# Performance work log

Measured on AMD Instinct MI355X. Metric: run time of the kernel, lower is better.

The kernel has to match this reference:

```python
import jax, jax.numpy as jnp
import numpy as np

B, n, A = 64, 1024, 32          # graphs, nodes/graph, actions/graph
N = B * n
EH = 2048                        # undirected edges per graph
HID, H = 128, 4
C = HID // H
NF, EF, AD, NI, L = 1, 1, 7, 4, 3
NEG_SLOPE = 0.2


def setup_inputs() -> dict:
    ks = jax.random.split(jax.random.key(0), 16)
    x = jax.random.normal(ks[0], (N, NF), jnp.float32)
    s = jax.random.randint(ks[1], (B, EH), 0, n)
    d = jax.random.randint(ks[2], (B, EH), 0, n)
    off = (jnp.arange(B) * n)[:, None]
    s = (s + off).reshape(-1)
    d = (d + off).reshape(-1)
    # bidirectional edges (unrooted trees): both i->j and j->i
    edge_index = jnp.stack([jnp.concatenate([s, d]), jnp.concatenate([d, s])]).astype(jnp.int32)
    E = edge_index.shape[1]
    edge_attr = jax.random.uniform(ks[3], (E, EF), jnp.float32)
    idx = jax.random.randint(ks[4], (B, A, NI), 0, n).astype(jnp.float32)
    meta = jax.random.normal(ks[5], (B, A, AD - NI), jnp.float32)
    action_tensor = jnp.concatenate([idx, meta], axis=-1)
    batch_idx = jnp.repeat(jnp.arange(B, dtype=jnp.int32), n)
    batch_ptr = jnp.arange(B + 1, dtype=jnp.int32) * n

    def lin(k, i, o):
        return jax.random.normal(k, (i, o), jnp.float32) / np.float32(np.sqrt(i))

    inp = dict(x=x, edge_attr=edge_attr, action_tensor=action_tensor,
               edge_index=edge_index, batch_idx=batch_idx, batch_ptr=batch_ptr)
    inp["Wn"] = lin(ks[6], NF, HID); inp["bn"] = jnp.zeros((HID,), jnp.float32)
    kl = jax.random.split(ks[7], 4 * L)
    inp["gWl"] = jnp.stack([lin(kl[i], HID, HID) for i in range(L)])
    inp["gWr"] = jnp.stack([lin(kl[L + i], HID, HID) for i in range(L)])
    inp["gWe"] = jnp.stack([lin(kl[2 * L + i], EF, HID) for i in range(L)])
    inp["gatt"] = jnp.stack([jax.random.normal(kl[3 * L + i], (H, C), jnp.float32) * 0.1 for i in range(L)])
    inp["gbl"] = jnp.zeros((L, HID), jnp.float32)
    inp["gbr"] = jnp.zeros((L, HID), jnp.float32)
    inp["gb"] = jnp.zeros((L, HID), jnp.float32)
    mlp_in = NI * HID + (AD - NI)
    inp["aW1"] = lin(ks[8], mlp_in, HID); inp["ab1"] = jnp.zeros((HID,), jnp.float32)
    inp["aW2"] = lin(ks[9], HID, HID); inp["ab2"] = jnp.zeros((HID,), jnp.float32)
    inp["qW1"] = lin(ks[10], 4 * HID, HID); inp["qb1"] = jnp.zeros((HID,), jnp.float32)
    inp["qW2"] = lin(ks[11], HID, HID); inp["qb2"] = jnp.zeros((HID,), jnp.float32)
    inp["qW3"] = lin(ks[12], HID, 1); inp["qb3"] = jnp.zeros((1,), jnp.float32)
    return inp


def _gatv2(h, src, dst, ea, Wl, bl, Wr, br, We, att, b):
    # PyG GATv2Conv: e_ij = att . leaky_relu(lin_l(x_j) + lin_r(x_i) + lin_edge(e_ij))
    Nn = h.shape[0]
    xl = (h @ Wl + bl).reshape(Nn, H, C)   # source transform
    xr = (h @ Wr + br).reshape(Nn, H, C)   # target transform
    ee = (ea @ We).reshape(-1, H, C)       # edge transform (no bias in PyG)
    e = jax.nn.leaky_relu(xl[src] + xr[dst] + ee, NEG_SLOPE)   # [E,H,C]
    logits = jnp.einsum('ehc,hc->eh', e, att)
    m = jax.ops.segment_max(logits, dst, num_segments=Nn)       # stable softmax per target node
    ex = jnp.exp(logits - m[dst])
    alpha = ex / jax.ops.segment_sum(ex, dst, num_segments=Nn)[dst]
    msg = (xl[src] * alpha[:, :, None]).reshape(-1, HID)
    return jax.ops.segment_sum(msg, dst, num_segments=Nn) + b


def reference(x, edge_attr, action_tensor, Wn, bn, gWl, gbl, gWr, gbr, gWe, gatt, gb,
              aW1, ab1, aW2, ab2, qW1, qb1, qW2, qb2, qW3, qb3,
              edge_index, batch_idx, batch_ptr):
    Nn = x.shape[0]
    nb = batch_ptr.shape[0] - 1
    # GATv2Conv default add_self_loops=True, fill_value='mean' for edge_attr
    loops = jnp.arange(Nn, dtype=edge_index.dtype)
    src = jnp.concatenate([edge_index[0], loops])
    dst = jnp.concatenate([edge_index[1], loops])
    ea = jnp.concatenate([edge_attr, jnp.broadcast_to(edge_attr.mean(0), (Nn, edge_attr.shape[1]))], 0)
    h = jax.nn.relu(x @ Wn + bn)
    for l in range(L):
        h = jax.nn.relu(_gatv2(h, src, dst, ea, gWl[l], gbl[l], gWr[l], gbr[l], gWe[l], gatt[l], gb[l])) + h
    # sum / mean / max pooling per graph
    sums = jax.ops.segment_sum(h, batch_idx, num_segments=nb)
    cnt = jax.ops.segment_sum(jnp.ones((Nn, 1), h.dtype), batch_idx, num_segments=nb)
    means = sums / cnt
    maxs = jax.ops.segment_max(h, batch_idx, num_segments=nb)
    tree_emb = jnp.concatenate([sums, means, maxs], -1)          # [B, 3*HID]
    # action encoding: gather node embeddings at action node indices (shifted by batch_ptr)
    ni = action_tensor[..., :NI].astype(jnp.int32) + batch_ptr[:-1][:, None, None]
    g = h[ni].reshape(nb, action_tensor.shape[1], NI * HID)
    ai = jnp.concatenate([g, action_tensor[..., NI:]], -1)
    ae = jax.nn.relu(jax.nn.relu(ai @ aW1 + ab1) @ aW2 + ab2)    # [B, A, HID]
    comb = jnp.concatenate([jnp.broadcast_to(tree_emb[:, None, :], (nb, ae.shape[1], 3 * HID)), ae], -1)
    q = jax.nn.relu(comb @ qW1 + qb1)
    q = jax.nn.relu(q @ qW2 + qb2)
    return (q @ qW3 + qb3).squeeze(-1)                            # [B, A]
```

## Files before the change

kernel.cpp:

```cpp
#include <hip/hip_runtime.h>
#include <hip/hip_bf16.h>

#define NNODES 65536
#define NGRAPH 64
#define NPG 1024
#define NACT 32
#define HID 128
#define DEGS 32

typedef __attribute__((ext_vector_type(8))) short bf16x8;
typedef __attribute__((ext_vector_type(4))) float f32x4;

__device__ __forceinline__ void load8(float* dst, const float* src) {
    float4 q0 = ((const float4*)src)[0];
    float4 q1 = ((const float4*)src)[1];
    dst[0]=q0.x; dst[1]=q0.y; dst[2]=q0.z; dst[3]=q0.w;
    dst[4]=q1.x; dst[5]=q1.y; dst[6]=q1.z; dst[7]=q1.w;
}

__device__ __forceinline__ void load8bf(float* dst, const unsigned short* src) {
    uint4 q = *(const uint4*)src;
    unsigned int u0 = q.x, u1 = q.y, u2 = q.z, u3 = q.w;
    dst[0] = __uint_as_float(u0 << 16); dst[1] = __uint_as_float(u0 & 0xffff0000u);
    dst[2] = __uint_as_float(u1 << 16); dst[3] = __uint_as_float(u1 & 0xffff0000u);
    dst[4] = __uint_as_float(u2 << 16); dst[5] = __uint_as_float(u2 & 0xffff0000u);
    dst[6] = __uint_as_float(u3 << 16); dst[7] = __uint_as_float(u3 & 0xffff0000u);
}

__device__ __forceinline__ unsigned short f2bf(float f) {
    unsigned int u = __float_as_uint(f);
    u = (u + 0x7fffu + ((u >> 16) & 1u)) >> 16;
    return (unsigned short)u;
}

__global__ void setup_k(const int* __restrict__ ei, const float* __restrict__ ea,
                        int* __restrict__ cursor, float* __restrict__ meansum,
                        int2* __restrict__ csr, int E0, int nsb,
                        const float* __restrict__ gWl, const float* __restrict__ gWr,
                        unsigned short* __restrict__ wtl, unsigned short* __restrict__ wtr,
                        const float* __restrict__ aW1, const float* __restrict__ aW2,
                        const float* __restrict__ qW1, const float* __restrict__ qW2,
                        unsigned short* __restrict__ wA1t, unsigned short* __restrict__ wA2t,
                        unsigned short* __restrict__ wQ1t, unsigned short* __restrict__ wQ2t) {
    int bid = blockIdx.x, t = threadIdx.x;
    if (bid < nsb) {
        __shared__ float s[256];
        int e = bid * 256 + t;
        float v = 0.f;
        if (e < E0) {
            int sn = ei[e], d = ei[E0 + e];
            int pos = atomicAdd(&cursor[d], 1);
            if (pos >= DEGS) pos = DEGS - 1;
            csr[(size_t)d * DEGS + pos] = make_int2(sn, __float_as_int(ea[e]));
            v = ea[e];
        }
        s[t] = v; __syncthreads();
        for (int off = 128; off > 0; off >>= 1) { if (t < off) s[t] += s[t+off]; __syncthreads(); }
        if (t == 0) atomicAdd(meansum, s[0]);
    } else if (bid < nsb + 192) {
        int idx = (bid - nsb) * 256 + t;
        int l = idx >> 14, rem = idx & 16383;
        int n = rem >> 7, k = rem & 127;
        int src = l*16384 + k*128 + n;
        wtl[idx] = f2bf(gWl[src]);
        wtr[idx] = f2bf(gWr[src]);
    } else {
        int n = bid - nsb - 192;
        for (int k = t; k < 544; k += 256)
            wA1t[n*544 + k] = (k < 515) ? f2bf(aW1[(size_t)k*128 + n]) : (unsigned short)0;
        if (t < 128) {
            wA2t[n*128 + t] = f2bf(aW2[(size_t)t*128 + n]);
            wQ1t[n*128 + t] = f2bf(qW1[(size_t)(384 + t)*128 + n]);
            wQ2t[n*128 + t] = f2bf(qW2[(size_t)t*128 + n]);
        }
    }
}

__global__ __launch_bounds__(256) void gemm_lr_mfma_k(
    const unsigned short* __restrict__ hb, const float* __restrict__ x,
    const float* __restrict__ Wn, const float* __restrict__ bn, int l0,
    const unsigned short* __restrict__ wtl, const unsigned short* __restrict__ wtr,
    const float* __restrict__ bl, const float* __restrict__ br,
    unsigned short* __restrict__ xlb, unsigned short* __restrict__ xrb) {
    int wave = threadIdx.x >> 6;
    int lane = threadIdx.x & 63;
    int lr = lane & 15;
    int lq = lane >> 4;
    int r0 = blockIdx.x * 128 + wave * 32;

    bf16x8 a[2][4];
    if (l0) {
        float xv0 = x[r0 + lr], xv1 = x[r0 + 16 + lr];
#pragma unroll
        for (int kf = 0; kf < 4; ++kf) {
            float wn[8], bv[8];
            load8(wn, Wn + kf*32 + lq*8);
            load8(bv, bn + kf*32 + lq*8);
            union { bf16x8 v; unsigned short u[8]; } p0, p1;
#pragma unroll
            for (int j = 0; j < 8; ++j) {
                p0.u[j] = f2bf(fmaxf(fmaf(xv0, wn[j], bv[j]), 0.f));
                p1.u[j] = f2bf(fmaxf(fmaf(xv1, wn[j], bv[j]), 0.f));
            }
            a[0][kf] = p0.v; a[1][kf] = p1.v;
        }
    } else {
        const short* hs = (const short*)hb;
#pragma unroll
        for (int rt = 0; rt < 2; ++rt)
#pragma unroll
            for (int kf = 0; kf < 4; ++kf)
                a[rt][kf] = *(const bf16x8*)(hs + (size_t)(r0 + rt*16 + lr)*HID + kf*32 + lq*8);
    }

    const short* ws[2]   = {(const short*)wtl, (const short*)wtr};
    const float* bias[2] = {bl, br};
    unsigned short* outp[2] = {xlb, xrb};

#pragma unroll
    for (int m = 0; m < 2; ++m) {
        const short* W = ws[m];
        f32x4 acc[2][8];
#pragma unroll
        for (int rt = 0; rt < 2; ++rt)
#pragma unroll
            for (int ct = 0; ct < 8; ++ct) acc[rt][ct] = (f32x4){0.f,0.f,0.f,0.f};

        bf16x8 b[4], nb[4];
#pragma unroll
        for (int kf = 0; kf < 4; ++kf)
            b[kf] = *(const bf16x8*)(W + (size_t)(lr)*HID + kf*32 + lq*8);
#pragma unroll
        for (int ct = 0; ct < 8; ++ct) {
            if (ct < 7) {
#pragma unroll
                for (int kf = 0; kf < 4; ++kf)
                    nb[kf] = *(const bf16x8*)(W + (size_t)((ct+1)*16 + lr)*HID + kf*32 + lq*8);
            }
#pragma unroll
            for (int rt = 0; rt < 2; ++rt)
#pragma unroll
                for (int kf = 0; kf < 4; ++kf)
                    acc[rt][ct] = __builtin_amdgcn_mfma_f32_16x16x32_bf16(a[rt][kf], b[kf], acc[rt][ct], 0, 0, 0);
#pragma unroll
            for (int kf = 0; kf < 4; ++kf) b[kf] = nb[kf];
        }
#pragma unroll
        for (int ct = 0; ct < 8; ++ct) {
            float bv = bias[m][ct*16 + lr];
#pragma unroll
            for (int rt = 0; rt < 2; ++rt)
#pragma unroll
                for (int rg = 0; rg < 4; ++rg) {
                    int row = r0 + rt*16 + lq*4 + rg;
                    outp[m][(size_t)row*HID + ct*16 + lr] = f2bf(acc[rt][ct][rg] + bv);
                }
        }
    }
}

__global__ __launch_bounds__(256, 4) void gat_edge_k(
    const unsigned short* __restrict__ xlb, const unsigned short* __restrict__ xrb,
    float* __restrict__ h, unsigned short* __restrict__ hb,
    const int* __restrict__ deg, const int2* __restrict__ csr,
    const float* __restrict__ We, const float* __restrict__ att,
    const float* __restrict__ gb, const float* __restrict__ meansum, float inv_e0,
    const float* __restrict__ x, const float* __restrict__ Wn, const float* __restrict__ bn,
    int l0, int do_pool, float* __restrict__ tree_sum, float* __restrict__ tree_max) {
    __shared__ float ps[16][132];
    __shared__ float pm[16][132];
    int xcd  = blockIdx.x & 7;
    int slot = blockIdx.x >> 3;
    int g    = xcd * 8 + (slot >> 6);
    int j    = slot & 63;
    int t    = threadIdx.x;
    int nd   = t >> 4;
    int v    = g * NPG + j * 16 + nd;
    int li   = t & 15;
    int base = li * 8;
    float mea = meansum[0] * inv_e0;

    float xrv[8], attv[8], wev[8];
    load8bf(xrv, xrb + (size_t)v*HID + base);
    load8(attv, att + base);
    load8(wev, We + base);

    float acc[8], xn[8];
    load8bf(xn, xlb + (size_t)v*HID + base);
    float m;
    {
        float lg = 0.f;
#pragma unroll
        for (int c = 0; c < 8; ++c) {
            float e = xn[c] + xrv[c] + mea * wev[c];
            e = fmaxf(e, 0.2f * e);
            lg = fmaf(attv[c], e, lg);
        }
        lg += __shfl_xor(lg, 1, 64);
        lg += __shfl_xor(lg, 2, 64);
        m = lg;
#pragma unroll
        for (int c = 0; c < 8; ++c) acc[c] = xn[c];
    }
    float den = 1.f;

    int dg = deg[v];
    if (dg > 0) {
        const int2* cp = csr + (size_t)v * DEGS;
        int2 ec = cp[0];
        int2 en = cp[dg > 1 ? 1 : 0];
        load8bf(xn, xlb + (size_t)ec.x*HID + base);
        for (int i = 0; i < dg; ++i) {
            int2 e3 = cp[(i + 2 < dg) ? i + 2 : dg - 1];
            float x2[8];
            load8bf(x2, xlb + (size_t)en.x*HID + base);
            float an = __int_as_float(ec.y);

            float lg = 0.f;
#pragma unroll
            for (int c = 0; c < 8; ++c) {
                float e = xn[c] + xrv[c] + an * wev[c];
                e = fmaxf(e, 0.2f * e);
                lg = fmaf(attv[c], e, lg);
            }
            lg += __shfl_xor(lg, 1, 64);
            lg += __shfl_xor(lg, 2, 64);

            float mn  = fmaxf(m, lg);
            float sc  = __expf(m - mn);
            float wgt = __expf(lg - mn);
            den = den * sc + wgt;
#pragma unroll
            for (int c = 0; c < 8; ++c) acc[c] = acc[c] * sc + wgt * xn[c];
            m = mn;
            ec = en; en = e3;
#pragma unroll
            for (int c = 0; c < 8; ++c) xn[c] = x2[c];
        }
    }

    float inv = 1.f / den;
    size_t o = (size_t)v*HID + base;
    float hold[8], gbv[8];
    if (l0) {
        float xv = x[v];
        float wn[8], bv[8];
        load8(wn, Wn + base);
        load8(bv, bn + base);
#pragma unroll
        for (int c = 0; c < 8; ++c) hold[c] = fmaxf(fmaf(xv, wn[c], bv[c]), 0.f);
    } else {
        load8(hold, h + o);
    }
    load8(gbv, gb + base);
    float nh[8];
#pragma unroll
    for (int c = 0; c < 8; ++c) {
        float val = acc[c] * inv + gbv[c];
        val = val > 0.f ? val : 0.f;
        nh[c] = val + hold[c];
    }
    float4* hp = (float4*)(h + o);
    hp[0] = make_float4(nh[0], nh[1], nh[2], nh[3]);
    hp[1] = make_float4(nh[4], nh[5], nh[6], nh[7]);
    unsigned int* hbp = (unsigned int*)(hb + o);
#pragma unroll
    for (int q = 0; q < 4; ++q)
        hbp[q] = (unsigned int)f2bf(nh[2*q]) | ((unsigned int)f2bf(nh[2*q+1]) << 16);

    if (do_pool) {
#pragma unroll
        for (int c = 0; c < 8; ++c) { ps[nd][base + c] = nh[c]; pm[nd][base + c] = nh[c]; }
        __syncthreads();
        if (t < 128) {
            float s = 0.f;
#pragma unroll
            for (int n = 0; n < 16; ++n) s += ps[n][t];
            atomicAdd(&tree_sum[g*128 + t], s);
        } else {
            int col = t - 128;
            float mx = 0.f;
#pragma unroll
            for (int n = 0; n < 16; ++n) mx = fmaxf(mx, pm[n][col]);
            atomicMax((int*)&tree_max[g*128 + col], __float_as_int(mx));
        }
    }
}

#define SA1 552
#define SAC 136
__global__ __launch_bounds__(256) void action_q_k(
    const unsigned short* __restrict__ hb, const float* __restrict__ action,
    const int* __restrict__ batch_ptr,
    const float* __restrict__ tree_sum, const float* __restrict__ tree_max,
    const unsigned short* __restrict__ wA1t, const float* __restrict__ ab1,
    const unsigned short* __restrict__ wA2t, const float* __restrict__ ab2,
    const float* __restrict__ qW1, const unsigned short* __restrict__ wQ1t,
    const float* __restrict__ qb1,
    const unsigned short* __restrict__ wQ2t, const float* __restrict__ qb2,
    const float* __restrict__ qW3, const float* __restrict__ qb3,
    float* __restrict__ out) {
    int b = blockIdx.x;
    int t = threadIdx.x;
    int w  = t >> 6;
    int lane = t & 63;
    int lr = lane & 15;
    int lq = lane >> 4;

    __shared__ unsigned short aib[32 * SA1];
    __shared__ unsigned short z1s[32 * SAC];
    __shared__ unsigned short aes[32 * SAC];
    __shared__ unsigned short q1s[32 * SAC];
    __shared__ float q2f[32 * 132];
    __shared__ float tqA[128], tqB[128];
    __shared__ float psum[32][8];

    int ptr = batch_ptr[b];

    {
        int p = t >> 1, half = t & 1;
        int a = p >> 2, j = p & 3;
        const float* actp = action + (size_t)(b * NACT + a) * 7;
        int ni = (int)actp[j] + ptr;
        const uint4* src = (const uint4*)(hb + (size_t)ni * HID) + half * 8;
        uint4* dst = (uint4*)((char*)aib + ((size_t)a * SA1 + j * 128 + half * 64) * 2);
#pragma unroll
        for (int q = 0; q < 8; ++q) dst[q] = src[q];
        if (t < 32) {
            const float* ap = action + (size_t)(b * NACT + t) * 7;
            aib[t * SA1 + 512] = f2bf(ap[4]);
            aib[t * SA1 + 513] = f2bf(ap[5]);
            aib[t * SA1 + 514] = f2bf(ap[6]);
            for (int i = 3; i < 40; ++i) aib[t * SA1 + 512 + i] = 0;
        }
    }

    {
        if (t < 128) {
            int col = t;
            float acc = 0.f;
#pragma unroll 4
            for (int k = 0; k < 128; ++k) {
                float sv = tree_sum[b * 128 + k];
                acc = fmaf(sv, qW1[(size_t)k * 128 + col], acc);
                acc = fmaf(sv * (1.f / 1024.f), qW1[(size_t)(128 + k) * 128 + col], acc);
            }
            tqA[col] = acc;
        } else {
            int col = t - 128;
            float acc = 0.f;
#pragma unroll 4
            for (int k = 0; k < 128; ++k) {
                float mv = tree_max[b * 128 + k];
                acc = fmaf(mv, qW1[(size_t)(256 + k) * 128 + col], acc);
            }
            tqB[col] = acc;
        }
    }
    __syncthreads();

    f32x4 acc[2][2];
    const unsigned short* srcA;
    int strideA, K;

    srcA = aib; strideA = SA1; K = 544;
#pragma unroll
    for (int rt = 0; rt < 2; ++rt)
#pragma unroll
        for (int ci = 0; ci < 2; ++ci) acc[rt][ci] = (f32x4){0.f, 0.f, 0.f, 0.f};
    for (int ks = 0; ks < K; ks += 32) {
        bf16x8 a0 = *(const bf16x8*)(srcA + (0 * 16 + lr) * strideA + ks + lq * 8);
        bf16x8 a1 = *(const bf16x8*)(srcA + (1 * 16 + lr) * strideA + ks + lq * 8);
        bf16x8 b0 = *(const bf16x8*)(wA1t + (size_t)((2 * w + 0) * 16 + lr) * K + ks + lq * 8);
        bf16x8 b1 = *(const bf16x8*)(wA1t + (size_t)((2 * w + 1) * 16 + lr) * K + ks + lq * 8);
        acc[0][0] = __builtin_amdgcn_mfma_f32_16x16x32_bf16(a0, b0, acc[0][0], 0, 0, 0);
        acc[0][1] = __builtin_amdgcn_mfma_f32_16x16x32_bf16(a0, b1, acc[0][1], 0, 0, 0);
        acc[1][0] = __builtin_amdgcn_mfma_f32_16x16x32_bf16(a1, b0, acc[1][0], 0, 0, 0);
        acc[1][1] = __builtin_amdgcn_mfma_f32_16x16x32_bf16(a1, b1, acc[1][1], 0, 0, 0);
    }
#pragma unroll
    for (int ci = 0; ci < 2; ++ci) {
        int col = (2 * w + ci) * 16 + lr;
        float bv = ab1[col];
#pragma unroll
        for (int rt = 0; rt < 2; ++rt)
#pragma unroll
            for (int rg = 0; rg < 4; ++rg) {
                int row = rt * 16 + lq * 4 + rg;
                z1s[row * SAC + col] = f2bf(fmaxf(acc[rt][ci][rg] + bv, 0.f));
            }
    }
    __syncthreads();

    srcA = z1s; strideA = SAC; K = 128;
#pragma unroll
    for (int rt = 0; rt < 2; ++rt)
#pragma unroll
        for (int ci = 0; ci < 2; ++ci) acc[rt][ci] = (f32x4){0.f, 0.f, 0.f, 0.f};
#pragma unroll
    for (int ks = 0; ks < 128; ks += 32) {
        bf16x8 a0 = *(const bf16x8*)(srcA + (0 * 16 + lr) * strideA + ks + lq * 8);
        bf16x8 a1 = *(const bf16x8*)(srcA + (1 * 16 + lr) * strideA + ks + lq * 8);
        bf16x8 b0 = *(const bf16x8*)(wA2t + (size_t)((2 * w + 0) * 16 + lr) * K + ks + lq * 8);
        bf16x8 b1 = *(const bf16x8*)(wA2t + (size_t)((2 * w + 1) * 16 + lr) * K + ks + lq * 8);
        acc[0][0] = __builtin_amdgcn_mfma_f32_16x16x32_bf16(a0, b0, acc[0][0], 0, 0, 0);
        acc[0][1] = __builtin_amdgcn_mfma_f32_16x16x32_bf16(a0, b1, acc[0][1], 0, 0, 0);
        acc[1][0] = __builtin_amdgcn_mfma_f32_16x16x32_bf16(a1, b0, acc[1][0], 0, 0, 0);
        acc[1][1] = __builtin_amdgcn_mfma_f32_16x16x32_bf16(a1, b1, acc[1][1], 0, 0, 0);
    }
#pragma unroll
    for (int ci = 0; ci < 2; ++ci) {
        int col = (2 * w + ci) * 16 + lr;
        float bv = ab2[col];
#pragma unroll
        for (int rt = 0; rt < 2; ++rt)
#pragma unroll
            for (int rg = 0; rg < 4; ++rg) {
                int row = rt * 16 + lq * 4 + rg;
                aes[row * SAC + col] = f2bf(fmaxf(acc[rt][ci][rg] + bv, 0.f));
            }
    }
    __syncthreads();

    srcA = aes; strideA = SAC; K = 128;
#pragma unroll
    for (int rt = 0; rt < 2; ++rt)
#pragma unroll
        for (int ci = 0; ci < 2; ++ci) acc[rt][ci] = (f32x4){0.f, 0.f, 0.f, 0.f};
#pragma unroll
    for (int ks = 0; ks < 128; ks += 32) {
        bf16x8 a0 = *(const bf16x8*)(srcA + (0 * 16 + lr) * strideA + ks + lq * 8);
        bf16x8 a1 = *(const bf16x8*)(srcA + (1 * 16 + lr) * strideA + ks + lq * 8);
        bf16x8 b0 = *(const bf16x8*)(wQ1t + (size_t)((2 * w + 0) * 16 + lr) * K + ks + lq * 8);
        bf16x8 b1 = *(const bf16x8*)(wQ1t + (size_t)((2 * w + 1) * 16 + lr) * K + ks + lq * 8);
        acc[0][0] = __builtin_amdgcn_mfma_f32_16x16x32_bf16(a0, b0, acc[0][0], 0, 0, 0);
        acc[0][1] = __builtin_amdgcn_mfma_f32_16x16x32_bf16(a0, b1, acc[0][1], 0, 0, 0);
        acc[1][0] = __builtin_amdgcn_mfma_f32_16x16x32_bf16(a1, b0, acc[1][0], 0, 0, 0);
        acc[1][1] = __builtin_amdgcn_mfma_f32_16x16x32_bf16(a1, b1, acc[1][1], 0, 0, 0);
    }
#pragma unroll
    for (int ci = 0; ci < 2; ++ci) {
        int col = (2 * w + ci) * 16 + lr;
        float bv = qb1[col] + tqA[col] + tqB[col];
#pragma unroll
        for (int rt = 0; rt < 2; ++rt)
#pragma unroll
            for (int rg = 0; rg < 4; ++rg) {
                int row = rt * 16 + lq * 4 + rg;
                q1s[row * SAC + col] = f2bf(fmaxf(acc[rt][ci][rg] + bv, 0.f));
            }
    }
    __syncthreads();

    srcA = q1s; strideA = SAC; K = 128;
#pragma unroll
    for (int rt = 0; rt < 2; ++rt)
#pragma unroll
        for (int ci = 0; ci < 2; ++ci) acc[rt][ci] = (f32x4){0.f, 0.f, 0.f, 0.f};
#pragma unroll
    for (int ks = 0; ks < 128; ks += 32) {
        bf16x8 a0 = *(const bf16x8*)(srcA + (0 * 16 + lr) * strideA + ks + lq * 8);
        bf16x8 a1 = *(const bf16x8*)(srcA + (1 * 16 + lr) * strideA + ks + lq * 8);
        bf16x8 b0 = *(const bf16x8*)(wQ2t + (size_t)((2 * w + 0) * 16 + lr) * K + ks + lq * 8);
        bf16x8 b1 = *(const bf16x8*)(wQ2t + (size_t)((2 * w + 1) * 16 + lr) * K + ks + lq * 8);
        acc[0][0] = __builtin_amdgcn_mfma_f32_16x16x32_bf16(a0, b0, acc[0][0], 0, 0, 0);
        acc[0][1] = __builtin_amdgcn_mfma_f32_16x16x32_bf16(a0, b1, acc[0][1], 0, 0, 0);
        acc[1][0] = __builtin_amdgcn_mfma_f32_16x16x32_bf16(a1, b0, acc[1][0], 0, 0, 0);
        acc[1][1] = __builtin_amdgcn_mfma_f32_16x16x32_bf16(a1, b1, acc[1][1], 0, 0, 0);
    }
#pragma unroll
    for (int ci = 0; ci < 2; ++ci) {
        int col = (2 * w + ci) * 16 + lr;
        float bv = qb2[col];
#pragma unroll
        for (int rt = 0; rt < 2; ++rt)
#pragma unroll
            for (int rg = 0; rg < 4; ++rg) {
                int row = rt * 16 + lq * 4 + rg;
                q2f[row * 132 + col] = fmaxf(acc[rt][ci][rg] + bv, 0.f);
            }
    }
    __syncthreads();

    {
        int a = t >> 3, seg = t & 7;
        float s = 0.f;
#pragma unroll
        for (int k = 0; k < 16; ++k)
            s = fmaf(q2f[a * 132 + seg * 16 + k], qW3[seg * 16 + k], s);
        psum[a][seg] = s;
    }
    __syncthreads();
    if (t < 32) {
        float s = qb3[0];
#pragma unroll
        for (int i = 0; i < 8; ++i) s += psum[t][i];
        out[(size_t)b * NACT + t] = s;
    }
}

extern "C" void kernel_launch(void* const* d_in, const int* in_sizes, int n_in,
                              void* d_out, int out_size, void* d_ws, size_t ws_size,
                              hipStream_t stream) {
    const float* x         = (const float*)d_in[0];
    const float* edge_attr = (const float*)d_in[1];
    const float* action    = (const float*)d_in[2];
    const int*   edge_idx  = (const int*)d_in[3];
    const int*   batch_ptr = (const int*)d_in[5];
    const float* Wn  = (const float*)d_in[6];
    const float* bn  = (const float*)d_in[7];
    const float* gWl = (const float*)d_in[8];
    const float* gWr = (const float*)d_in[9];
    const float* gWe = (const float*)d_in[10];
    const float* gatt= (const float*)d_in[11];
    const float* gbl = (const float*)d_in[12];
    const float* gbr = (const float*)d_in[13];
    const float* gb  = (const float*)d_in[14];
    const float* aW1 = (const float*)d_in[15];
    const float* ab1 = (const float*)d_in[16];
    const float* aW2 = (const float*)d_in[17];
    const float* ab2 = (const float*)d_in[18];
    const float* qW1 = (const float*)d_in[19];
    const float* qb1 = (const float*)d_in[20];
    const float* qW2 = (const float*)d_in[21];
    const float* qb2 = (const float*)d_in[22];
    const float* qW3 = (const float*)d_in[23];
    const float* qb3 = (const float*)d_in[24];
    float* out = (float*)d_out;

    const int E0 = in_sizes[1];
    const int N  = NNODES;

    char* w = (char*)d_ws;
    auto alloc = [&](size_t bytes) { void* p = (void*)w; w += (bytes + 255) & ~(size_t)255; return p; };
    float* h        = (float*)alloc((size_t)N * HID * 4);
    unsigned short* hb  = (unsigned short*)alloc((size_t)N * HID * 2);
    unsigned short* xlb = (unsigned short*)alloc((size_t)N * HID * 2);
    unsigned short* xrb = (unsigned short*)alloc((size_t)N * HID * 2);
    int2*  csr      = (int2*)alloc((size_t)N * DEGS * 8);
    int*   cursor   = (int*)alloc((size_t)N * 4);
    float* meansum  = (float*)alloc(256);
    float* tree_sum = (float*)alloc((size_t)NGRAPH * 128 * 4);
    float* tree_max = (float*)alloc((size_t)NGRAPH * 128 * 4);
    size_t zero_span = (size_t)((char*)(tree_max + NGRAPH * 128) - (char*)cursor);
    unsigned short* wtl = (unsigned short*)alloc((size_t)3*128*128*2);
    unsigned short* wtr = (unsigned short*)alloc((size_t)3*128*128*2);
    unsigned short* wA1t = (unsigned short*)alloc((size_t)128*544*2);
    unsigned short* wA2t = (unsigned short*)alloc((size_t)128*128*2);
    unsigned short* wQ1t = (unsigned short*)alloc((size_t)128*128*2);
    unsigned short* wQ2t = (unsigned short*)alloc((size_t)128*128*2);

    hipMemsetAsync(cursor, 0, zero_span, stream);

    int nsb = (E0 + 255) / 256;
    setup_k<<<nsb + 320, 256, 0, stream>>>(edge_idx, edge_attr, cursor, meansum, csr, E0, nsb,
                                           gWl, gWr, wtl, wtr,
                                           aW1, aW2, qW1, qW2, wA1t, wA2t, wQ1t, wQ2t);

    float inv_e0 = 1.0f / (float)E0;
    for (int l = 0; l < 3; ++l) {
        gemm_lr_mfma_k<<<N / 128, 256, 0, stream>>>(
            hb, x, Wn, bn, (l == 0) ? 1 : 0,
            wtl + (size_t)l*128*128, wtr + (size_t)l*128*128,
            gbl + l*HID, gbr + l*HID, xlb, xrb);
        gat_edge_k<<<N / 16, 256, 0, stream>>>(
            xlb, xrb, h, hb, cursor, csr,
            gWe + l*HID, gatt + l*128, gb + l*HID, meansum, inv_e0,
            x, Wn, bn, (l == 0) ? 1 : 0, (l == 2) ? 1 : 0, tree_sum, tree_max);
    }

    action_q_k<<<NGRAPH, 256, 0, stream>>>(
        hb, action, batch_ptr, tree_sum, tree_max,
        wA1t, ab1, wA2t, ab2, qW1, wQ1t, qb1, wQ2t, qb2, qW3, qb3, out);
}
```

Measured before the change: 315.6 us.

## Drop fp32 hidden state, keep residual in bf16, deepen neighbor prefetch to two

Removes the fp32 copy of the node hidden state. The residual is now read from the bf16 buffer instead, which cuts per-layer global reads and writes of h roughly in half. The neighbor gather loop now prefetches features two edges ahead instead of one, to hide gather latency, and the degree is clamped to the CSR capacity. The risk is that residual accumulation across layers now goes through bf16 rounding, which lowers precision, and the extra prefetch buffer adds register pressure.

```diff
diff --git a/kernel.cpp b/kernel.cpp
--- a/kernel.cpp
+++ b/kernel.cpp
@@ -161,7 +161,7 @@
 
 __global__ __launch_bounds__(256, 4) void gat_edge_k(
     const unsigned short* __restrict__ xlb, const unsigned short* __restrict__ xrb,
-    float* __restrict__ h, unsigned short* __restrict__ hb,
+    unsigned short* __restrict__ hb,
     const int* __restrict__ deg, const int2* __restrict__ csr,
     const float* __restrict__ We, const float* __restrict__ att,
     const float* __restrict__ gb, const float* __restrict__ meansum, float inv_e0,
@@ -185,14 +185,14 @@
     load8(attv, att + base);
     load8(wev, We + base);
 
-    float acc[8], xn[8];
-    load8bf(xn, xlb + (size_t)v*HID + base);
+    float acc[8], xA[8];
+    load8bf(xA, xlb + (size_t)v*HID + base);
     float m;
     {
         float lg = 0.f;
 #pragma unroll
         for (int c = 0; c < 8; ++c) {
-            float e = xn[c] + xrv[c] + mea * wev[c];
+            float e = xA[c] + xrv[c] + mea * wev[c];
             e = fmaxf(e, 0.2f * e);
             lg = fmaf(attv[c], e, lg);
         }
@@ -200,26 +200,29 @@
         lg += __shfl_xor(lg, 2, 64);
         m = lg;
 #pragma unroll
-        for (int c = 0; c < 8; ++c) acc[c] = xn[c];
+        for (int c = 0; c < 8; ++c) acc[c] = xA[c];
     }
     float den = 1.f;
 
     int dg = deg[v];
+    if (dg > DEGS) dg = DEGS;
     if (dg > 0) {
         const int2* cp = csr + (size_t)v * DEGS;
-        int2 ec = cp[0];
-        int2 en = cp[dg > 1 ? 1 : 0];
-        load8bf(xn, xlb + (size_t)ec.x*HID + base);
+        int2 e0 = cp[0];
+        int2 e1 = cp[(1 < dg) ? 1 : dg - 1];
+        float xB[8];
+        load8bf(xA, xlb + (size_t)e0.x*HID + base);
+        load8bf(xB, xlb + (size_t)e1.x*HID + base);
         for (int i = 0; i < dg; ++i) {
-            int2 e3 = cp[(i + 2 < dg) ? i + 2 : dg - 1];
-            float x2[8];
-            load8bf(x2, xlb + (size_t)en.x*HID + base);
-            float an = __int_as_float(ec.y);
+            int2 e2 = cp[(i + 2 < dg) ? i + 2 : dg - 1];
+            float xC[8];
+            load8bf(xC, xlb + (size_t)e2.x*HID + base);
+            float an = __int_as_float(e0.y);
 
             float lg = 0.f;
 #pragma unroll
             for (int c = 0; c < 8; ++c) {
-                float e = xn[c] + xrv[c] + an * wev[c];
+                float e = xA[c] + xrv[c] + an * wev[c];
                 e = fmaxf(e, 0.2f * e);
                 lg = fmaf(attv[c], e, lg);
             }
@@ -231,11 +234,11 @@
             float wgt = __expf(lg - mn);
             den = den * sc + wgt;
 #pragma unroll
-            for (int c = 0; c < 8; ++c) acc[c] = acc[c] * sc + wgt * xn[c];
+            for (int c = 0; c < 8; ++c) acc[c] = acc[c] * sc + wgt * xA[c];
             m = mn;
-            ec = en; en = e3;
-#pragma unroll
-            for (int c = 0; c < 8; ++c) xn[c] = x2[c];
+            e0 = e1; e1 = e2;
+#pragma unroll
+            for (int c = 0; c < 8; ++c) { xA[c] = xB[c]; xB[c] = xC[c]; }
         }
     }
 
@@ -250,7 +253,7 @@
 #pragma unroll
         for (int c = 0; c < 8; ++c) hold[c] = fmaxf(fmaf(xv, wn[c], bv[c]), 0.f);
     } else {
-        load8(hold, h + o);
+        load8bf(hold, hb + o);
     }
     load8(gbv, gb + base);
     float nh[8];
@@ -260,9 +263,6 @@
         val = val > 0.f ? val : 0.f;
         nh[c] = val + hold[c];
     }
-    float4* hp = (float4*)(h + o);
-    hp[0] = make_float4(nh[0], nh[1], nh[2], nh[3]);
-    hp[1] = make_float4(nh[4], nh[5], nh[6], nh[7]);
     unsigned int* hbp = (unsigned int*)(hb + o);
 #pragma unroll
     for (int q = 0; q < 4; ++q)
@@ -533,7 +533,6 @@
 
     char* w = (char*)d_ws;
     auto alloc = [&](size_t bytes) { void* p = (void*)w; w += (bytes + 255) & ~(size_t)255; return p; };
-    float* h        = (float*)alloc((size_t)N * HID * 4);
     unsigned short* hb  = (unsigned short*)alloc((size_t)N * HID * 2);
     unsigned short* xlb = (unsigned short*)alloc((size_t)N * HID * 2);
     unsigned short* xrb = (unsigned short*)alloc((size_t)N * HID * 2);
@@ -564,7 +563,7 @@
             wtl + (size_t)l*128*128, wtr + (size_t)l*128*128,
             gbl + l*HID, gbr + l*HID, xlb, xrb);
         gat_edge_k<<<N / 16, 256, 0, stream>>>(
-            xlb, xrb, h, hb, cursor, csr,
+            xlb, xrb, hb, cursor, csr,
             gWe + l*HID, gatt + l*128, gb + l*HID, meansum, inv_e0,
             x, Wn, bn, (l == 0) ? 1 : 0, (l == 2) ? 1 : 0, tree_sum, tree_max);
     }
```

Measured after the change: 310.3 us. No clear change (-1.7%).
